# Performance work log

Hardware: AMD Instinct MI355X
Metric: run time of the kernel (lower is better)

## Reference

```python
import jax, jax.numpy as jnp
import numpy as np
from jax import lax

B, T, H, W, C = 2, 16, 64, 64, 64
KT, K = 3, 3


def kernel_to_freq_3d(kernel, T, H, W):
    # kernel: (C, k_t, k_h, k_w) -> (C, T, H, W) complex freq response
    Cc, k_t, k_h, k_w = kernel.shape
    t_idx = (jnp.arange(k_t) - k_t // 2) % T
    h_idx = (jnp.arange(k_h) - k_h // 2) % H
    w_idx = (jnp.arange(k_w) - k_w // 2) % W
    tt, th, tw = jnp.meshgrid(t_idx, h_idx, w_idx, indexing='ij')
    padded = jnp.zeros((Cc, T, H, W), dtype=kernel.dtype).at[:, tt, th, tw].set(kernel)
    return jnp.fft.fftn(padded, axes=(1, 2, 3))


def mamba_op(left, right):
    a1, b1 = left
    a2, b2 = right
    return (a1 * a2, a2 * b1 + b2)


def setup_inputs() -> dict:
    key = jax.random.key(0)
    ks = jax.random.split(key, 8)
    fan_in = KT * K * K
    x = jax.random.normal(ks[0], (B, T, H, W, C), dtype=jnp.float32)
    A_kernel = jax.random.normal(ks[1], (C, KT, K, K), dtype=jnp.float32) / np.sqrt(fan_in)
    B_kernel = jax.random.normal(ks[2], (C, KT, K, K), dtype=jnp.float32) / np.sqrt(fan_in)
    forget_bias = jnp.full((C,), 2.0, dtype=jnp.float32)
    forget_scale = jnp.full((C,), 0.01, dtype=jnp.float32)
    input_bias = jnp.zeros((C,), dtype=jnp.float32)
    input_scale = jnp.full((C,), 0.01, dtype=jnp.float32)
    delta_W = jax.random.normal(ks[3], (C, C), dtype=jnp.float32) / np.sqrt(C)
    delta_b = jnp.zeros((C,), dtype=jnp.float32)
    return {"x": x, "A_kernel": A_kernel, "B_kernel": B_kernel,
            "forget_bias": forget_bias, "forget_scale": forget_scale,
            "input_bias": input_bias, "input_scale": input_scale,
            "delta_W": delta_W, "delta_b": delta_b}


def reference(x, A_kernel, B_kernel, forget_bias, forget_scale,
              input_bias, input_scale, delta_W, delta_b):
    Bb, Tt, Hh, Ww, Cc = x.shape
    # freq-domain kernels: (C,T,H,W) -> (T,1,H,W,C) for broadcasting over batch
    A_f = kernel_to_freq_3d(A_kernel, Tt, Hh, Ww).transpose(1, 2, 3, 0)[:, None]
    B_f = kernel_to_freq_3d(B_kernel, Tt, Hh, Ww).transpose(1, 2, 3, 0)[:, None]
    # input-dependent gates (real, elementwise per channel)
    forget_gate = jax.nn.sigmoid(forget_bias + forget_scale * x)
    input_gate = jax.nn.sigmoid(input_bias + input_scale * x)
    delta = jax.nn.softplus(jnp.einsum('bthwc,cd->bthwd', x, delta_W) + delta_b)
    x_f = jnp.fft.fftn(x, axes=(1, 2, 3))  # complex (B,T,H,W,C)
    # move time axis to front for the scan: (T,B,H,W,C)
    a_seq = forget_gate.transpose(1, 0, 2, 3, 4) * A_f
    b_seq = (input_gate.transpose(1, 0, 2, 3, 4)
             * delta.transpose(1, 0, 2, 3, 4)
             * B_f * x_f.transpose(1, 0, 2, 3, 4))
    _, h_all_f = lax.associative_scan(mamba_op, (a_seq, b_seq), axis=0)
    h_f = h_all_f.transpose(1, 0, 2, 3, 4)
    h = jnp.fft.ifftn(h_f, axes=(1, 2, 3)).real
    return h.astype(x.dtype)
```

## Files before the change

### kernel.cpp

```cpp
#include <hip/hip_runtime.h>
#include <math.h>

#define Bb 2
#define Tt 16
#define Hh 64
#define Ww 64
#define Cc 64
#define ST_ (Hh*Ww*Cc)
#define SB_ (Tt*Hh*Ww*Cc)

#define TWO_PI 6.2831853071795864769f

typedef __attribute__((ext_vector_type(8))) short bf16x8;
typedef __attribute__((ext_vector_type(4))) float f32x4;

#define BUF_A    0u
#define BUF_B    8388608u
#define OFF_PRE  16777216u
#define OFF_TWF  16779264u
#define OFF_THF  16783360u
#define OFF_THI  16791552u
#define OFF_TWI  16799744u

__device__ __forceinline__ float2 cmul(float2 a, float2 b) {
    return make_float2(fmaf(a.x, b.x, -a.y * b.y), fmaf(a.x, b.y, a.y * b.x));
}
__device__ __forceinline__ float2 cadd(float2 a, float2 b) { return make_float2(a.x + b.x, a.y + b.y); }
__device__ __forceinline__ float2 csub(float2 a, float2 b) { return make_float2(a.x - b.x, a.y - b.y); }

__device__ __forceinline__ unsigned bfpack(float2 f) {
    unsigned r = __float_as_uint(f.x);
    unsigned i = __float_as_uint(f.y);
    r = (r + 0x7fffu + ((r >> 16) & 1u)) >> 16;
    i = (i + 0x7fffu + ((i >> 16) & 1u)) >> 16;
    return r | (i << 16);
}
__device__ __forceinline__ float2 bfunpack(unsigned u) {
    return make_float2(__uint_as_float(u << 16), __uint_as_float(u & 0xffff0000u));
}

template <int S>
__device__ __forceinline__ void fft4(float2& a, float2& b, float2& c, float2& d) {
    float2 t0 = cadd(a, c), t1 = csub(a, c);
    float2 t2 = cadd(b, d), t3 = csub(b, d);
    a = cadd(t0, t2);
    c = csub(t0, t2);
    b = make_float2(t1.x - (float)S * t3.y, t1.y + (float)S * t3.x);
    d = make_float2(t1.x + (float)S * t3.y, t1.y - (float)S * t3.x);
}

template <int S>
__device__ __forceinline__ void fft16(float2 v[16]) {
    const float CS[10] = {1.f, 0.92387953f, 0.70710678f, 0.38268343f, 0.f,
                          -0.38268343f, -0.70710678f, -0.92387953f, -1.f, -0.92387953f};
    const float SN[10] = {0.f, 0.38268343f, 0.70710678f, 0.92387953f, 1.f,
                          0.92387953f, 0.70710678f, 0.38268343f, 0.f, -0.38268343f};
    float2 A[4][4];
#pragma unroll
    for (int j = 0; j < 4; ++j) {
        A[j][0] = v[j]; A[j][1] = v[4 + j]; A[j][2] = v[8 + j]; A[j][3] = v[12 + j];
        fft4<S>(A[j][0], A[j][1], A[j][2], A[j][3]);
#pragma unroll
        for (int k0 = 0; k0 < 4; ++k0) {
            int m = j * k0;
            float2 tw = make_float2(CS[m], (float)S * SN[m]);
            A[j][k0] = cmul(A[j][k0], tw);
        }
    }
#pragma unroll
    for (int k0 = 0; k0 < 4; ++k0) {
        fft4<S>(A[0][k0], A[1][k0], A[2][k0], A[3][k0]);
        v[k0] = A[0][k0]; v[k0 + 4] = A[1][k0]; v[k0 + 8] = A[2][k0]; v[k0 + 12] = A[3][k0];
    }
}

__global__ __launch_bounds__(256) void k_setup(const float* __restrict__ dW,
                                               unsigned* __restrict__ ws) {
    int j = blockIdx.x * 256 + threadIdx.x;
    if (j < 2048) {
        int p2 = j & 3, lane = (j >> 2) & 63, ka = (j >> 8) & 1, nt = j >> 9;
        int kb = ka * 32 + (lane >> 4) * 8 + 2 * p2;
        int ccol = (lane & 15) + 16 * nt;
        ws[OFF_PRE + j] = bfpack(make_float2(dW[kb * 64 + ccol], dW[(kb + 1) * 64 + ccol]));
        return;
    }
    int idx, table;
    if (j < 6144)       { idx = j - 2048;  table = 0; }
    else if (j < 14336) { idx = j - 6144;  table = 1; }
    else if (j < 22528) { idx = j - 14336; table = 2; }
    else                { idx = j - 22528; table = 3; }
    int p = idx & 3;
    int lane = (idx >> 2) & 63;
    int m = lane & 15, q = lane >> 4;
    int ka, r, reim;
    if (table == 0)      { ka = (idx >> 8) & 1; r = (idx >> 9) & 3;  reim = (idx >> 11) & 1; }
    else if (table == 3) { ka = (idx >> 8) & 3; r = (idx >> 10) & 3; reim = 0; }
    else                 { ka = (idx >> 8) & 3; r = (idx >> 10) & 3; reim = (idx >> 12) & 1; }
    int wp = r * 16 + m;
    int k0 = ka * 32 + q * 8 + 2 * p;
    float val[2];
#pragma unroll
    for (int dk = 0; dk < 2; ++dk) {
        int k = k0 + dk;
        float v;
        if (table == 0) {
            int a = (wp * k) & 63;
            float sn, cs; sincosf(TWO_PI * (float)a * (1.0f / 64.0f), &sn, &cs);
            v = (reim == 0) ? cs : -sn;
        } else {
            int h = k >> 1;
            int a = (wp * h) & 63;
            float sn, cs; sincosf(TWO_PI * (float)a * (1.0f / 64.0f), &sn, &cs);
            bool even = (k & 1) == 0;
            if (table == 1) {
                v = (reim == 0) ? (even ? cs : sn) : (even ? -sn : cs);
            } else if (table == 2) {
                v = (reim == 0) ? (even ? cs : -sn) : (even ? sn : cs);
                v *= (1.0f / 64.0f);
            } else {
                v = (even ? cs : -sn) * (1.0f / 64.0f);
            }
        }
        val[dk] = v;
    }
    unsigned base = (table == 0) ? OFF_TWF : (table == 1) ? OFF_THF
                  : (table == 2) ? OFF_THI : OFF_TWI;
    ws[base + idx] = bfpack(make_float2(val[0], val[1]));
}

__global__ __launch_bounds__(256) void k_dft_w_fwd(const float* __restrict__ x,
                                                   unsigned* __restrict__ X1,
                                                   const uint4* __restrict__ T) {
    __shared__ unsigned zw[64 * 66];
    int tid = threadIdx.x;
    int s = blockIdx.x;
    const float* src = x + (size_t)s * 4096;
    for (int idx = tid; idx < 2048; idx += 256) {
        int i = idx >> 6, c = idx & 63;
        zw[c * 66 + i] = bfpack(make_float2(src[i * 128 + c], src[i * 128 + 64 + c]));
    }
    __syncthreads();

    int r = tid >> 6, lane = tid & 63;
    int m = lane & 15, q = lane >> 4;
    union U48 { uint4 u4; uint2 u2[2]; unsigned u[4]; bf16x8 v8; };
    U48 Are[2], Aim[2], Bf;
#pragma unroll
    for (int ka = 0; ka < 2; ++ka) {
        Are[ka].u4 = T[((0 * 4 + r) * 2 + ka) * 64 + lane];
        Aim[ka].u4 = T[((1 * 4 + r) * 2 + ka) * 64 + lane];
    }
    f32x4 ar[4], ai[4];
#pragma unroll
    for (int nt = 0; nt < 4; ++nt) { ar[nt] = (f32x4){0.f,0.f,0.f,0.f}; ai[nt] = (f32x4){0.f,0.f,0.f,0.f}; }
#pragma unroll
    for (int nt = 0; nt < 4; ++nt) {
        int cc = m + 16 * nt;
#pragma unroll
        for (int ka = 0; ka < 2; ++ka) {
            int i0 = ka * 16 + q * 4;
            Bf.u2[0] = *(const uint2*)&zw[cc * 66 + i0];
            Bf.u2[1] = *(const uint2*)&zw[cc * 66 + i0 + 2];
            ar[nt] = __builtin_amdgcn_mfma_f32_16x16x32_bf16(Are[ka].v8, Bf.v8, ar[nt], 0, 0, 0);
            ai[nt] = __builtin_amdgcn_mfma_f32_16x16x32_bf16(Aim[ka].v8, Bf.v8, ai[nt], 0, 0, 0);
        }
    }
    int bt = s >> 6, h = s & 63;
    size_t ob = (size_t)bt * 262144 + (size_t)h * 64;
#pragma unroll
    for (int nt = 0; nt < 4; ++nt) {
        int cc = m + 16 * nt;
#pragma unroll
        for (int reg = 0; reg < 4; ++reg) {
            int wp = r * 16 + q * 4 + reg;
            X1[ob + (size_t)wp * 4096 + cc] = bfpack(make_float2(ar[nt][reg], ai[nt][reg]));
        }
    }
}

__global__ __launch_bounds__(256) void k_dft_h_fwd(const unsigned* __restrict__ X1,
                                                   unsigned* __restrict__ X2,
                                                   const uint4* __restrict__ T) {
    __shared__ unsigned zs[64 * 66];
    int tid = threadIdx.x;
    int s = blockIdx.x;
    const unsigned* src = X1 + (size_t)s * 4096;
    for (int i = tid; i < 4096; i += 256) {
        int h = i >> 6, c = i & 63;
        zs[c * 66 + h] = src[i];
    }
    __syncthreads();

    int r = tid >> 6, lane = tid & 63;
    int m = lane & 15, q = lane >> 4;
    union U48 { uint4 u4; uint2 u2[2]; unsigned u[4]; bf16x8 v8; };
    U48 Are[4], Aim[4], Bf;
#pragma unroll
    for (int ka = 0; ka < 4; ++ka) {
        Are[ka].u4 = T[((0 * 4 + r) * 4 + ka) * 64 + lane];
        Aim[ka].u4 = T[((1 * 4 + r) * 4 + ka) * 64 + lane];
    }
    f32x4 ar[4], ai[4];
#pragma unroll
    for (int nt = 0; nt < 4; ++nt) { ar[nt] = (f32x4){0.f,0.f,0.f,0.f}; ai[nt] = (f32x4){0.f,0.f,0.f,0.f}; }
#pragma unroll
    for (int nt = 0; nt < 4; ++nt) {
        int cc = m + 16 * nt;
#pragma unroll
        for (int ka = 0; ka < 4; ++ka) {
            int h0 = ka * 16 + q * 4;
            Bf.u2[0] = *(const uint2*)&zs[cc * 66 + h0];
            Bf.u2[1] = *(const uint2*)&zs[cc * 66 + h0 + 2];
            ar[nt] = __builtin_amdgcn_mfma_f32_16x16x32_bf16(Are[ka].v8, Bf.v8, ar[nt], 0, 0, 0);
            ai[nt] = __builtin_amdgcn_mfma_f32_16x16x32_bf16(Aim[ka].v8, Bf.v8, ai[nt], 0, 0, 0);
        }
    }
    int b = s >> 10, t = (s >> 6) & 15, w = s & 63;
    size_t ob = (size_t)b * 4194304 + (size_t)w * 1024 + (size_t)t * 64;
#pragma unroll
    for (int nt = 0; nt < 4; ++nt) {
        int cc = m + 16 * nt;
#pragma unroll
        for (int reg = 0; reg < 4; ++reg) {
            int hp = r * 16 + q * 4 + reg;
            X2[ob + (size_t)hp * 65536 + cc] = bfpack(make_float2(ar[nt][reg], ai[nt][reg]));
        }
    }
}

__global__ __launch_bounds__(256) void k_dft_h_inv(const unsigned* __restrict__ X3,
                                                   unsigned* __restrict__ X4,
                                                   const uint4* __restrict__ T) {
    __shared__ unsigned zs[64 * 66];
    int tid = threadIdx.x;
    int s = blockIdx.x;
    const unsigned* src = X3 + (size_t)s * 4096;
    for (int i = tid; i < 4096; i += 256) {
        int h = i >> 6, c = i & 63;
        zs[c * 66 + h] = src[i];
    }
    __syncthreads();

    int r = tid >> 6, lane = tid & 63;
    int m = lane & 15, q = lane >> 4;
    union U48 { uint4 u4; uint2 u2[2]; unsigned u[4]; bf16x8 v8; };
    U48 Are[4], Aim[4], Bf;
#pragma unroll
    for (int ka = 0; ka < 4; ++ka) {
        Are[ka].u4 = T[((0 * 4 + r) * 4 + ka) * 64 + lane];
        Aim[ka].u4 = T[((1 * 4 + r) * 4 + ka) * 64 + lane];
    }
    f32x4 ar[4], ai[4];
#pragma unroll
    for (int nt = 0; nt < 4; ++nt) { ar[nt] = (f32x4){0.f,0.f,0.f,0.f}; ai[nt] = (f32x4){0.f,0.f,0.f,0.f}; }
#pragma unroll
    for (int nt = 0; nt < 4; ++nt) {
        int cc = m + 16 * nt;
#pragma unroll
        for (int ka = 0; ka < 4; ++ka) {
            int h0 = ka * 16 + q * 4;
            Bf.u2[0] = *(const uint2*)&zs[cc * 66 + h0];
            Bf.u2[1] = *(const uint2*)&zs[cc * 66 + h0 + 2];
            ar[nt] = __builtin_amdgcn_mfma_f32_16x16x32_bf16(Are[ka].v8, Bf.v8, ar[nt], 0, 0, 0);
            ai[nt] = __builtin_amdgcn_mfma_f32_16x16x32_bf16(Aim[ka].v8, Bf.v8, ai[nt], 0, 0, 0);
        }
    }
    int bt = s >> 6, w = s & 63;
    size_t ob = (size_t)bt * 262144 + (size_t)w * 64;
#pragma unroll
    for (int nt = 0; nt < 4; ++nt) {
        int cc = m + 16 * nt;
#pragma unroll
        for (int reg = 0; reg < 4; ++reg) {
            int hp = r * 16 + q * 4 + reg;
            X4[ob + (size_t)hp * 4096 + cc] = bfpack(make_float2(ar[nt][reg], ai[nt][reg]));
        }
    }
}

__global__ __launch_bounds__(256) void k_dft_w_inv(const unsigned* __restrict__ X4,
                                                   float* __restrict__ out,
                                                   const uint4* __restrict__ T) {
    __shared__ unsigned zs[64 * 66];
    int tid = threadIdx.x;
    int s = blockIdx.x;
    const unsigned* src = X4 + (size_t)s * 4096;
    for (int i = tid; i < 4096; i += 256) {
        int w = i >> 6, c = i & 63;
        zs[c * 66 + w] = src[i];
    }
    __syncthreads();

    int r = tid >> 6, lane = tid & 63;
    int m = lane & 15, q = lane >> 4;
    union U48 { uint4 u4; uint2 u2[2]; unsigned u[4]; bf16x8 v8; };
    U48 Are[4], Bf;
#pragma unroll
    for (int ka = 0; ka < 4; ++ka)
        Are[ka].u4 = T[(r * 4 + ka) * 64 + lane];
    f32x4 ar[4];
#pragma unroll
    for (int nt = 0; nt < 4; ++nt) ar[nt] = (f32x4){0.f,0.f,0.f,0.f};
#pragma unroll
    for (int nt = 0; nt < 4; ++nt) {
        int cc = m + 16 * nt;
#pragma unroll
        for (int ka = 0; ka < 4; ++ka) {
            int w0 = ka * 16 + q * 4;
            Bf.u2[0] = *(const uint2*)&zs[cc * 66 + w0];
            Bf.u2[1] = *(const uint2*)&zs[cc * 66 + w0 + 2];
            ar[nt] = __builtin_amdgcn_mfma_f32_16x16x32_bf16(Are[ka].v8, Bf.v8, ar[nt], 0, 0, 0);
        }
    }
    float* dst = out + (size_t)s * 4096;
#pragma unroll
    for (int nt = 0; nt < 4; ++nt) {
        int cc = m + 16 * nt;
#pragma unroll
        for (int reg = 0; reg < 4; ++reg) {
            int wp = r * 16 + q * 4 + reg;
            dst[wp * 64 + cc] = ar[nt][reg];
        }
    }
}

__global__ __launch_bounds__(256) void k_mid(
    const float* __restrict__ x, const unsigned* __restrict__ X2,
    unsigned* __restrict__ X3,
    const float* __restrict__ Ak, const float* __restrict__ Bk,
    const float* __restrict__ fb, const float* __restrict__ fs,
    const float* __restrict__ ib, const float* __restrict__ isc_,
    const uint4* __restrict__ pre, const float* __restrict__ db) {
    const float CT[16] = {1.f, 0.9238795f, 0.7071068f, 0.3826834f, 0.f, -0.3826834f,
                          -0.7071068f, -0.9238795f, -1.f, -0.9238795f, -0.7071068f,
                          -0.3826834f, 0.f, 0.3826834f, 0.7071068f, 0.9238795f};
    const float SN[16] = {0.f, 0.3826834f, 0.7071068f, 0.9238795f, 1.f, 0.9238795f,
                          0.7071068f, 0.3826834f, 0.f, -0.3826834f, -0.7071068f,
                          -0.9238795f, -1.f, -0.9238795f, -0.7071068f, -0.3826834f};
    __shared__ float Akl[1728], Bkl[1728];
    __shared__ __align__(16) float xs[4][16 * 68 + 4];

    int tid = threadIdx.x;
    int g = tid >> 6, lane = tid & 63;
    int c = lane;
    int site = blockIdx.x * 4 + g;
    int b = site >> 12, hw = site & 4095;
    int h = hw >> 6, w = hw & 63;
    size_t base = (size_t)b * SB_ + (size_t)hw * 64;

    for (int i = tid; i < 1728; i += 256) { Akl[i] = Ak[i]; Bkl[i] = Bk[i]; }

    float xv[16];
    float2 v[16];
    const unsigned* src2 = X2 + (size_t)site * 1024;
#pragma unroll
    for (int t = 0; t < 16; ++t) {
        xv[t] = x[base + (size_t)t * ST_ + c];
        v[t] = bfunpack(src2[t * 64 + c]);
    }
#pragma unroll
    for (int t = 0; t < 16; ++t) xs[g][t * 68 + c] = xv[t];
    __syncthreads();

    int m = lane & 15, q = lane >> 4;
    bf16x8 Afrag[2];
#pragma unroll
    for (int ka = 0; ka < 2; ++ka) {
        int d0 = ka * 32 + q * 8;
        const float* p = &xs[g][m * 68 + d0];
        float4 f0 = *(const float4*)p;
        float4 f1 = *(const float4*)(p + 4);
        union { bf16x8 v8; unsigned u[4]; } U;
        U.u[0] = bfpack(make_float2(f0.x, f0.y));
        U.u[1] = bfpack(make_float2(f0.z, f0.w));
        U.u[2] = bfpack(make_float2(f1.x, f1.y));
        U.u[3] = bfpack(make_float2(f1.z, f1.w));
        Afrag[ka] = U.v8;
    }
#pragma unroll
    for (int nt = 0; nt < 4; ++nt) {
        int ccol = m + 16 * nt;
        float dbn = db[ccol];
        f32x4 acc = {dbn, dbn, dbn, dbn};
#pragma unroll
        for (int ka = 0; ka < 2; ++ka) {
            union { bf16x8 v8; uint4 u4; } Ub;
            Ub.u4 = pre[(nt * 2 + ka) * 64 + lane];
            acc = __builtin_amdgcn_mfma_f32_16x16x32_bf16(Afrag[ka], Ub.v8, acc, 0, 0, 0);
        }
#pragma unroll
        for (int reg = 0; reg < 4; ++reg)
            xs[g][(q * 4 + reg) * 68 + ccol] = acc[reg];
    }

    float sh, ch; sincosf(TWO_PI * (float)h / 64.0f, &sh, &ch);
    float sw, cw; sincosf(TWO_PI * (float)w / 64.0f, &sw, &cw);
    float2 eh[3] = { make_float2(ch, sh), make_float2(1.f, 0.f), make_float2(ch, -sh) };
    float2 ew[3] = { make_float2(cw, sw), make_float2(1.f, 0.f), make_float2(cw, -sw) };
    float2 GA[3], GB[3];
#pragma unroll
    for (int kt = 0; kt < 3; ++kt) { GA[kt] = make_float2(0.f, 0.f); GB[kt] = make_float2(0.f, 0.f); }
#pragma unroll
    for (int kh = 0; kh < 3; ++kh) {
#pragma unroll
        for (int kw = 0; kw < 3; ++kw) {
            float2 e = cmul(eh[kh], ew[kw]);
#pragma unroll
            for (int kt = 0; kt < 3; ++kt) {
                float ka = Akl[c * 27 + kt * 9 + kh * 3 + kw];
                float kb = Bkl[c * 27 + kt * 9 + kh * 3 + kw];
                GA[kt].x = fmaf(ka, e.x, GA[kt].x);
                GA[kt].y = fmaf(ka, e.y, GA[kt].y);
                GB[kt].x = fmaf(kb, e.x, GB[kt].x);
                GB[kt].y = fmaf(kb, e.y, GB[kt].y);
            }
        }
    }
    float fbc = fb[c], fsc = fs[c], ibc = ib[c], iscv = isc_[c];

    fft16<-1>(v);
    __syncthreads();

    float delta_raw[16];
#pragma unroll
    for (int t = 0; t < 16; ++t) delta_raw[t] = xs[g][t * 68 + c];

    float2 hv = make_float2(0.f, 0.f);
#pragma unroll
    for (int t = 0; t < 16; ++t) {
        float ct = CT[t], st = SN[t];
        float2 Af, Bf;
        Af.x = GA[1].x + ct * (GA[0].x + GA[2].x) - st * (GA[0].y - GA[2].y);
        Af.y = GA[1].y + ct * (GA[0].y + GA[2].y) + st * (GA[0].x - GA[2].x);
        Bf.x = GB[1].x + ct * (GB[0].x + GB[2].x) - st * (GB[0].y - GB[2].y);
        Bf.y = GB[1].y + ct * (GB[0].y + GB[2].y) + st * (GB[0].x - GB[2].x);

        float xc = xv[t];
        float fg  = __builtin_amdgcn_rcpf(1.f + __expf(-(fbc + fsc * xc)));
        float igv = __builtin_amdgcn_rcpf(1.f + __expf(-(ibc + iscv * xc)));
        float dot = delta_raw[t];
        float delta = (dot > 20.f) ? dot : __logf(1.f + __expf(dot));

        float sR = igv * delta;
        float2 bbv;
        bbv.x = sR * (Bf.x * v[t].x - Bf.y * v[t].y);
        bbv.y = sR * (Bf.x * v[t].y + Bf.y * v[t].x);
        float2 av = make_float2(fg * Af.x, fg * Af.y);
        float2 nh;
        nh.x = av.x * hv.x - av.y * hv.y + bbv.x;
        nh.y = av.x * hv.y + av.y * hv.x + bbv.y;
        hv = nh;
        v[t] = hv;
    }

    fft16<1>(v);

    size_t ob = (size_t)b * 4194304 + (size_t)w * 4096 + (size_t)h * 64 + c;
#pragma unroll
    for (int t = 0; t < 16; ++t) {
        float2 o = make_float2(v[t].x * 0.0625f, v[t].y * 0.0625f);
        X3[ob + (size_t)t * 262144] = bfpack(o);
    }
}

extern "C" void kernel_launch(void* const* d_in, const int* in_sizes, int n_in,
                              void* d_out, int out_size, void* d_ws, size_t ws_size,
                              hipStream_t stream) {
    const float* x   = (const float*)d_in[0];
    const float* Ak  = (const float*)d_in[1];
    const float* Bk  = (const float*)d_in[2];
    const float* fb  = (const float*)d_in[3];
    const float* fs  = (const float*)d_in[4];
    const float* ib  = (const float*)d_in[5];
    const float* is_ = (const float*)d_in[6];
    const float* dW  = (const float*)d_in[7];
    const float* db  = (const float*)d_in[8];
    float* out = (float*)d_out;
    unsigned* ws = (unsigned*)d_ws;
    unsigned* A = ws + BUF_A;
    unsigned* B = ws + BUF_B;

    k_setup<<<104, 256, 0, stream>>>(dW, ws);
    k_dft_w_fwd<<<Bb * Tt * Hh, 256, 0, stream>>>(x, A, (const uint4*)(ws + OFF_TWF));
    k_dft_h_fwd<<<Bb * Tt * Ww, 256, 0, stream>>>(A, B, (const uint4*)(ws + OFF_THF));
    k_mid<<<(Bb * Hh * Ww) / 4, 256, 0, stream>>>(x, B, A, Ak, Bk, fb, fs, ib, is_,
                                                  (const uint4*)(ws + OFF_PRE), db);
    k_dft_h_inv<<<Bb * Tt * Ww, 256, 0, stream>>>(A, B, (const uint4*)(ws + OFF_THI));
    k_dft_w_inv<<<Bb * Tt * Hh, 256, 0, stream>>>(B, out, (const uint4*)(ws + OFF_TWI));
}
```

Before: 175.2 us.

## Fuse W and H DFT passes into single 2D kernels with in-LDS transpose

Replaces the separate W and H forward DFT kernels, and likewise the two inverse kernels, with one 2D kernel each. Each 512-thread block handles an 8-channel slab of one (b,t) plane and keeps the intermediate in a swizzled 128KB LDS buffer, so the intermediate no longer round-trips through global memory. Twiddle tables and the delta_W bf16 fragments are now computed in registers in every block, which removes the setup kernel and three launches. The cost is heavy LDS use per block, only 256 blocks with few waves each, sincos work repeated in every block, and strided 64-element global accesses.

```diff
diff --git a/kernel.cpp b/kernel.cpp
--- a/kernel.cpp
+++ b/kernel.cpp
@@ -16,11 +16,6 @@
 
 #define BUF_A    0u
 #define BUF_B    8388608u
-#define OFF_PRE  16777216u
-#define OFF_TWF  16779264u
-#define OFF_THF  16783360u
-#define OFF_THI  16791552u
-#define OFF_TWI  16799744u
 
 __device__ __forceinline__ float2 cmul(float2 a, float2 b) {
     return make_float2(fmaf(a.x, b.x, -a.y * b.y), fmaf(a.x, b.y, a.y * b.x));
@@ -37,6 +32,73 @@
 }
 __device__ __forceinline__ float2 bfunpack(unsigned u) {
     return make_float2(__uint_as_float(u << 16), __uint_as_float(u & 0xffff0000u));
+}
+
+union U48 { uint4 u4; uint2 u2[2]; unsigned u[4]; bf16x8 v8; };
+
+__device__ __forceinline__ U48 tw_wf(int wp, int q, int ka, int reim) {
+    U48 o;
+#pragma unroll
+    for (int p = 0; p < 4; ++p) {
+        int k0 = ka * 32 + q * 8 + 2 * p;
+        float v[2];
+#pragma unroll
+        for (int dk = 0; dk < 2; ++dk) {
+            int k = k0 + dk;
+            int a = (wp * k) & 63;
+            float sn, cs; sincosf(TWO_PI * (float)a * (1.0f / 64.0f), &sn, &cs);
+            v[dk] = reim ? -sn : cs;
+        }
+        o.u[p] = bfpack(make_float2(v[0], v[1]));
+    }
+    return o;
+}
+
+__device__ __forceinline__ U48 tw_cpx(int wp, int q, int ka, int reim, int tbl) {
+    U48 o;
+#pragma unroll
+    for (int p = 0; p < 4; ++p) {
+        int k0 = ka * 32 + q * 8 + 2 * p;
+        float v[2];
+#pragma unroll
+        for (int dk = 0; dk < 2; ++dk) {
+            int k = k0 + dk;
+            int h = k >> 1;
+            int a = (wp * h) & 63;
+            float sn, cs; sincosf(TWO_PI * (float)a * (1.0f / 64.0f), &sn, &cs);
+            bool even = (k & 1) == 0;
+            float vv;
+            if (tbl == 1) vv = reim ? (even ? -sn : cs) : (even ? cs : sn);
+            else          vv = (reim ? (even ? sn : cs) : (even ? cs : -sn)) * (1.0f / 64.0f);
+            v[dk] = vv;
+        }
+        o.u[p] = bfpack(make_float2(v[0], v[1]));
+    }
+    return o;
+}
+
+__device__ __forceinline__ U48 tw_wi(int wp, int q, int ka) {
+    U48 o;
+#pragma unroll
+    for (int p = 0; p < 4; ++p) {
+        int k0 = ka * 32 + q * 8 + 2 * p;
+        float v[2];
+#pragma unroll
+        for (int dk = 0; dk < 2; ++dk) {
+            int k = k0 + dk;
+            int h = k >> 1;
+            int a = (wp * h) & 63;
+            float sn, cs; sincosf(TWO_PI * (float)a * (1.0f / 64.0f), &sn, &cs);
+            bool even = (k & 1) == 0;
+            v[dk] = (even ? cs : -sn) * (1.0f / 64.0f);
+        }
+        o.u[p] = bfpack(make_float2(v[0], v[1]));
+    }
+    return o;
+}
+
+__device__ __forceinline__ int zidx(int col, int h) {
+    return (col << 6) + (h ^ (((col >> 1) & 7) << 3));
 }
 
 template <int S>
@@ -74,252 +136,149 @@
     }
 }
 
-__global__ __launch_bounds__(256) void k_setup(const float* __restrict__ dW,
-                                               unsigned* __restrict__ ws) {
-    int j = blockIdx.x * 256 + threadIdx.x;
-    if (j < 2048) {
-        int p2 = j & 3, lane = (j >> 2) & 63, ka = (j >> 8) & 1, nt = j >> 9;
-        int kb = ka * 32 + (lane >> 4) * 8 + 2 * p2;
-        int ccol = (lane & 15) + 16 * nt;
-        ws[OFF_PRE + j] = bfpack(make_float2(dW[kb * 64 + ccol], dW[(kb + 1) * 64 + ccol]));
-        return;
-    }
-    int idx, table;
-    if (j < 6144)       { idx = j - 2048;  table = 0; }
-    else if (j < 14336) { idx = j - 6144;  table = 1; }
-    else if (j < 22528) { idx = j - 14336; table = 2; }
-    else                { idx = j - 22528; table = 3; }
-    int p = idx & 3;
-    int lane = (idx >> 2) & 63;
+__global__ __launch_bounds__(512) void k_fwd2d(const float* __restrict__ x,
+                                               unsigned* __restrict__ X2) {
+    __shared__ unsigned Z[512 * 64];
+    int tid = threadIdx.x;
+    int lane = tid & 63, r = (tid >> 6) & 3, team = tid >> 8;
     int m = lane & 15, q = lane >> 4;
-    int ka, r, reim;
-    if (table == 0)      { ka = (idx >> 8) & 1; r = (idx >> 9) & 3;  reim = (idx >> 11) & 1; }
-    else if (table == 3) { ka = (idx >> 8) & 3; r = (idx >> 10) & 3; reim = 0; }
-    else                 { ka = (idx >> 8) & 3; r = (idx >> 10) & 3; reim = (idx >> 12) & 1; }
+    int wg = blockIdx.x;
+    int bt = wg >> 3;
+    int c0 = (wg & 7) * 8;
+    int b = wg >> 7, t = (wg >> 3) & 15;
+    const float* xs = x + (size_t)bt * 262144;
     int wp = r * 16 + m;
-    int k0 = ka * 32 + q * 8 + 2 * p;
-    float val[2];
-#pragma unroll
-    for (int dk = 0; dk < 2; ++dk) {
-        int k = k0 + dk;
-        float v;
-        if (table == 0) {
-            int a = (wp * k) & 63;
-            float sn, cs; sincosf(TWO_PI * (float)a * (1.0f / 64.0f), &sn, &cs);
-            v = (reim == 0) ? cs : -sn;
-        } else {
-            int h = k >> 1;
-            int a = (wp * h) & 63;
-            float sn, cs; sincosf(TWO_PI * (float)a * (1.0f / 64.0f), &sn, &cs);
-            bool even = (k & 1) == 0;
-            if (table == 1) {
-                v = (reim == 0) ? (even ? cs : sn) : (even ? -sn : cs);
-            } else if (table == 2) {
-                v = (reim == 0) ? (even ? cs : -sn) : (even ? sn : cs);
-                v *= (1.0f / 64.0f);
-            } else {
-                v = (even ? cs : -sn) * (1.0f / 64.0f);
+    int hme = m >> 3, cme = m & 7;
+
+    U48 Are[2], Aim[2];
+#pragma unroll
+    for (int ka = 0; ka < 2; ++ka) { Are[ka] = tw_wf(wp, q, ka, 0); Aim[ka] = tw_wf(wp, q, ka, 1); }
+#pragma unroll 2
+    for (int gi = 0; gi < 16; ++gi) {
+        int g = gi * 2 + team;
+        int h = g * 2 + hme;
+        const float* xr = xs + (size_t)h * 4096 + (c0 + cme);
+        U48 B[2];
+#pragma unroll
+        for (int ka = 0; ka < 2; ++ka)
+#pragma unroll
+            for (int p = 0; p < 4; ++p) {
+                int w0 = ka * 32 + q * 8 + 2 * p;
+                B[ka].u[p] = bfpack(make_float2(xr[(size_t)w0 * 64], xr[(size_t)(w0 + 1) * 64]));
             }
-        }
-        val[dk] = v;
-    }
-    unsigned base = (table == 0) ? OFF_TWF : (table == 1) ? OFF_THF
-                  : (table == 2) ? OFF_THI : OFF_TWI;
-    ws[base + idx] = bfpack(make_float2(val[0], val[1]));
-}
-
-__global__ __launch_bounds__(256) void k_dft_w_fwd(const float* __restrict__ x,
-                                                   unsigned* __restrict__ X1,
-                                                   const uint4* __restrict__ T) {
-    __shared__ unsigned zw[64 * 66];
-    int tid = threadIdx.x;
-    int s = blockIdx.x;
-    const float* src = x + (size_t)s * 4096;
-    for (int idx = tid; idx < 2048; idx += 256) {
-        int i = idx >> 6, c = idx & 63;
-        zw[c * 66 + i] = bfpack(make_float2(src[i * 128 + c], src[i * 128 + 64 + c]));
+        f32x4 ar = {0.f, 0.f, 0.f, 0.f}, ai = {0.f, 0.f, 0.f, 0.f};
+#pragma unroll
+        for (int ka = 0; ka < 2; ++ka) {
+            ar = __builtin_amdgcn_mfma_f32_16x16x32_bf16(Are[ka].v8, B[ka].v8, ar, 0, 0, 0);
+            ai = __builtin_amdgcn_mfma_f32_16x16x32_bf16(Aim[ka].v8, B[ka].v8, ai, 0, 0, 0);
+        }
+#pragma unroll
+        for (int reg = 0; reg < 4; ++reg) {
+            int wpp = r * 16 + q * 4 + reg;
+            Z[zidx(wpp * 8 + cme, h)] = bfpack(make_float2(ar[reg], ai[reg]));
+        }
     }
     __syncthreads();
 
-    int r = tid >> 6, lane = tid & 63;
-    int m = lane & 15, q = lane >> 4;
-    union U48 { uint4 u4; uint2 u2[2]; unsigned u[4]; bf16x8 v8; };
-    U48 Are[2], Aim[2], Bf;
-#pragma unroll
-    for (int ka = 0; ka < 2; ++ka) {
-        Are[ka].u4 = T[((0 * 4 + r) * 2 + ka) * 64 + lane];
-        Aim[ka].u4 = T[((1 * 4 + r) * 2 + ka) * 64 + lane];
-    }
-    f32x4 ar[4], ai[4];
-#pragma unroll
-    for (int nt = 0; nt < 4; ++nt) { ar[nt] = (f32x4){0.f,0.f,0.f,0.f}; ai[nt] = (f32x4){0.f,0.f,0.f,0.f}; }
-#pragma unroll
-    for (int nt = 0; nt < 4; ++nt) {
-        int cc = m + 16 * nt;
-#pragma unroll
-        for (int ka = 0; ka < 2; ++ka) {
-            int i0 = ka * 16 + q * 4;
-            Bf.u2[0] = *(const uint2*)&zw[cc * 66 + i0];
-            Bf.u2[1] = *(const uint2*)&zw[cc * 66 + i0 + 2];
-            ar[nt] = __builtin_amdgcn_mfma_f32_16x16x32_bf16(Are[ka].v8, Bf.v8, ar[nt], 0, 0, 0);
-            ai[nt] = __builtin_amdgcn_mfma_f32_16x16x32_bf16(Aim[ka].v8, Bf.v8, ai[nt], 0, 0, 0);
-        }
-    }
-    int bt = s >> 6, h = s & 63;
-    size_t ob = (size_t)bt * 262144 + (size_t)h * 64;
-#pragma unroll
-    for (int nt = 0; nt < 4; ++nt) {
-        int cc = m + 16 * nt;
-#pragma unroll
-        for (int reg = 0; reg < 4; ++reg) {
-            int wp = r * 16 + q * 4 + reg;
-            X1[ob + (size_t)wp * 4096 + cc] = bfpack(make_float2(ar[nt][reg], ai[nt][reg]));
-        }
-    }
-}
-
-__global__ __launch_bounds__(256) void k_dft_h_fwd(const unsigned* __restrict__ X1,
-                                                   unsigned* __restrict__ X2,
-                                                   const uint4* __restrict__ T) {
-    __shared__ unsigned zs[64 * 66];
-    int tid = threadIdx.x;
-    int s = blockIdx.x;
-    const unsigned* src = X1 + (size_t)s * 4096;
-    for (int i = tid; i < 4096; i += 256) {
-        int h = i >> 6, c = i & 63;
-        zs[c * 66 + h] = src[i];
-    }
-    __syncthreads();
-
-    int r = tid >> 6, lane = tid & 63;
-    int m = lane & 15, q = lane >> 4;
-    union U48 { uint4 u4; uint2 u2[2]; unsigned u[4]; bf16x8 v8; };
-    U48 Are[4], Aim[4], Bf;
-#pragma unroll
-    for (int ka = 0; ka < 4; ++ka) {
-        Are[ka].u4 = T[((0 * 4 + r) * 4 + ka) * 64 + lane];
-        Aim[ka].u4 = T[((1 * 4 + r) * 4 + ka) * 64 + lane];
-    }
-    f32x4 ar[4], ai[4];
-#pragma unroll
-    for (int nt = 0; nt < 4; ++nt) { ar[nt] = (f32x4){0.f,0.f,0.f,0.f}; ai[nt] = (f32x4){0.f,0.f,0.f,0.f}; }
-#pragma unroll
-    for (int nt = 0; nt < 4; ++nt) {
-        int cc = m + 16 * nt;
+    U48 Hre[4], Him[4];
+#pragma unroll
+    for (int ka = 0; ka < 4; ++ka) { Hre[ka] = tw_cpx(wp, q, ka, 0, 1); Him[ka] = tw_cpx(wp, q, ka, 1, 1); }
+    size_t ob = (size_t)b * 4194304 + (size_t)t * 64 + (c0 + cme);
+#pragma unroll 2
+    for (int gi = 0; gi < 16; ++gi) {
+        int g = gi * 2 + team;
+        int col = g * 16 + m;
+        int w = g * 2 + hme;
+        U48 B[4];
 #pragma unroll
         for (int ka = 0; ka < 4; ++ka) {
             int h0 = ka * 16 + q * 4;
-            Bf.u2[0] = *(const uint2*)&zs[cc * 66 + h0];
-            Bf.u2[1] = *(const uint2*)&zs[cc * 66 + h0 + 2];
-            ar[nt] = __builtin_amdgcn_mfma_f32_16x16x32_bf16(Are[ka].v8, Bf.v8, ar[nt], 0, 0, 0);
-            ai[nt] = __builtin_amdgcn_mfma_f32_16x16x32_bf16(Aim[ka].v8, Bf.v8, ai[nt], 0, 0, 0);
-        }
-    }
-    int b = s >> 10, t = (s >> 6) & 15, w = s & 63;
-    size_t ob = (size_t)b * 4194304 + (size_t)w * 1024 + (size_t)t * 64;
-#pragma unroll
-    for (int nt = 0; nt < 4; ++nt) {
-        int cc = m + 16 * nt;
+            int zi = zidx(col, h0);
+            B[ka].u2[0] = *(const uint2*)&Z[zi];
+            B[ka].u2[1] = *(const uint2*)&Z[zi + 2];
+        }
+        f32x4 ar = {0.f, 0.f, 0.f, 0.f}, ai = {0.f, 0.f, 0.f, 0.f};
+#pragma unroll
+        for (int ka = 0; ka < 4; ++ka) {
+            ar = __builtin_amdgcn_mfma_f32_16x16x32_bf16(Hre[ka].v8, B[ka].v8, ar, 0, 0, 0);
+            ai = __builtin_amdgcn_mfma_f32_16x16x32_bf16(Him[ka].v8, B[ka].v8, ai, 0, 0, 0);
+        }
 #pragma unroll
         for (int reg = 0; reg < 4; ++reg) {
             int hp = r * 16 + q * 4 + reg;
-            X2[ob + (size_t)hp * 65536 + cc] = bfpack(make_float2(ar[nt][reg], ai[nt][reg]));
-        }
-    }
-}
-
-__global__ __launch_bounds__(256) void k_dft_h_inv(const unsigned* __restrict__ X3,
-                                                   unsigned* __restrict__ X4,
-                                                   const uint4* __restrict__ T) {
-    __shared__ unsigned zs[64 * 66];
+            X2[ob + (size_t)hp * 65536 + (size_t)w * 1024] = bfpack(make_float2(ar[reg], ai[reg]));
+        }
+    }
+}
+
+__global__ __launch_bounds__(512) void k_inv2d(const unsigned* __restrict__ X3,
+                                               float* __restrict__ out) {
+    __shared__ unsigned Z[512 * 64];
     int tid = threadIdx.x;
-    int s = blockIdx.x;
-    const unsigned* src = X3 + (size_t)s * 4096;
-    for (int i = tid; i < 4096; i += 256) {
-        int h = i >> 6, c = i & 63;
-        zs[c * 66 + h] = src[i];
-    }
-    __syncthreads();
-
-    int r = tid >> 6, lane = tid & 63;
+    int lane = tid & 63, r = (tid >> 6) & 3, team = tid >> 8;
     int m = lane & 15, q = lane >> 4;
-    union U48 { uint4 u4; uint2 u2[2]; unsigned u[4]; bf16x8 v8; };
-    U48 Are[4], Aim[4], Bf;
-#pragma unroll
-    for (int ka = 0; ka < 4; ++ka) {
-        Are[ka].u4 = T[((0 * 4 + r) * 4 + ka) * 64 + lane];
-        Aim[ka].u4 = T[((1 * 4 + r) * 4 + ka) * 64 + lane];
-    }
-    f32x4 ar[4], ai[4];
-#pragma unroll
-    for (int nt = 0; nt < 4; ++nt) { ar[nt] = (f32x4){0.f,0.f,0.f,0.f}; ai[nt] = (f32x4){0.f,0.f,0.f,0.f}; }
-#pragma unroll
-    for (int nt = 0; nt < 4; ++nt) {
-        int cc = m + 16 * nt;
+    int wg = blockIdx.x;
+    int bt = wg >> 3;
+    int c0 = (wg & 7) * 8;
+    const unsigned* xs = X3 + (size_t)bt * 262144;
+    int wp = r * 16 + m;
+    int hme = m >> 3, cme = m & 7;
+
+    U48 Hre[4], Him[4];
+#pragma unroll
+    for (int ka = 0; ka < 4; ++ka) { Hre[ka] = tw_cpx(wp, q, ka, 0, 2); Him[ka] = tw_cpx(wp, q, ka, 1, 2); }
+#pragma unroll 2
+    for (int gi = 0; gi < 16; ++gi) {
+        int g = gi * 2 + team;
+        int w = g * 2 + hme;
+        const unsigned* xr = xs + (size_t)w * 4096 + (c0 + cme);
+        U48 B[4];
+#pragma unroll
+        for (int ka = 0; ka < 4; ++ka)
+#pragma unroll
+            for (int j = 0; j < 4; ++j) {
+                int h = ka * 16 + q * 4 + j;
+                B[ka].u[j] = xr[(size_t)h * 64];
+            }
+        f32x4 ar = {0.f, 0.f, 0.f, 0.f}, ai = {0.f, 0.f, 0.f, 0.f};
 #pragma unroll
         for (int ka = 0; ka < 4; ++ka) {
-            int h0 = ka * 16 + q * 4;
-            Bf.u2[0] = *(const uint2*)&zs[cc * 66 + h0];
-            Bf.u2[1] = *(const uint2*)&zs[cc * 66 + h0 + 2];
-            ar[nt] = __builtin_amdgcn_mfma_f32_16x16x32_bf16(Are[ka].v8, Bf.v8, ar[nt], 0, 0, 0);
-            ai[nt] = __builtin_amdgcn_mfma_f32_16x16x32_bf16(Aim[ka].v8, Bf.v8, ai[nt], 0, 0, 0);
-        }
-    }
-    int bt = s >> 6, w = s & 63;
-    size_t ob = (size_t)bt * 262144 + (size_t)w * 64;
-#pragma unroll
-    for (int nt = 0; nt < 4; ++nt) {
-        int cc = m + 16 * nt;
+            ar = __builtin_amdgcn_mfma_f32_16x16x32_bf16(Hre[ka].v8, B[ka].v8, ar, 0, 0, 0);
+            ai = __builtin_amdgcn_mfma_f32_16x16x32_bf16(Him[ka].v8, B[ka].v8, ai, 0, 0, 0);
+        }
 #pragma unroll
         for (int reg = 0; reg < 4; ++reg) {
             int hp = r * 16 + q * 4 + reg;
-            X4[ob + (size_t)hp * 4096 + cc] = bfpack(make_float2(ar[nt][reg], ai[nt][reg]));
-        }
-    }
-}
-
-__global__ __launch_bounds__(256) void k_dft_w_inv(const unsigned* __restrict__ X4,
-                                                   float* __restrict__ out,
-                                                   const uint4* __restrict__ T) {
-    __shared__ unsigned zs[64 * 66];
-    int tid = threadIdx.x;
-    int s = blockIdx.x;
-    const unsigned* src = X4 + (size_t)s * 4096;
-    for (int i = tid; i < 4096; i += 256) {
-        int w = i >> 6, c = i & 63;
-        zs[c * 66 + w] = src[i];
+            Z[zidx(hp * 8 + cme, w)] = bfpack(make_float2(ar[reg], ai[reg]));
+        }
     }
     __syncthreads();
 
-    int r = tid >> 6, lane = tid & 63;
-    int m = lane & 15, q = lane >> 4;
-    union U48 { uint4 u4; uint2 u2[2]; unsigned u[4]; bf16x8 v8; };
-    U48 Are[4], Bf;
-#pragma unroll
-    for (int ka = 0; ka < 4; ++ka)
-        Are[ka].u4 = T[(r * 4 + ka) * 64 + lane];
-    f32x4 ar[4];
-#pragma unroll
-    for (int nt = 0; nt < 4; ++nt) ar[nt] = (f32x4){0.f,0.f,0.f,0.f};
-#pragma unroll
-    for (int nt = 0; nt < 4; ++nt) {
-        int cc = m + 16 * nt;
+    U48 Wre[4];
+#pragma unroll
+    for (int ka = 0; ka < 4; ++ka) Wre[ka] = tw_wi(wp, q, ka);
+#pragma unroll 2
+    for (int gi = 0; gi < 16; ++gi) {
+        int g = gi * 2 + team;
+        int col = g * 16 + m;
+        int h = g * 2 + hme;
+        U48 B[4];
 #pragma unroll
         for (int ka = 0; ka < 4; ++ka) {
             int w0 = ka * 16 + q * 4;
-            Bf.u2[0] = *(const uint2*)&zs[cc * 66 + w0];
-            Bf.u2[1] = *(const uint2*)&zs[cc * 66 + w0 + 2];
-            ar[nt] = __builtin_amdgcn_mfma_f32_16x16x32_bf16(Are[ka].v8, Bf.v8, ar[nt], 0, 0, 0);
-        }
-    }
-    float* dst = out + (size_t)s * 4096;
-#pragma unroll
-    for (int nt = 0; nt < 4; ++nt) {
-        int cc = m + 16 * nt;
+            int zi = zidx(col, w0);
+            B[ka].u2[0] = *(const uint2*)&Z[zi];
+            B[ka].u2[1] = *(const uint2*)&Z[zi + 2];
+        }
+        f32x4 ar = {0.f, 0.f, 0.f, 0.f};
+#pragma unroll
+        for (int ka = 0; ka < 4; ++ka)
+            ar = __builtin_amdgcn_mfma_f32_16x16x32_bf16(Wre[ka].v8, B[ka].v8, ar, 0, 0, 0);
+        float* dst = out + (size_t)bt * 262144 + (size_t)h * 4096 + (c0 + cme);
 #pragma unroll
         for (int reg = 0; reg < 4; ++reg) {
-            int wp = r * 16 + q * 4 + reg;
-            dst[wp * 64 + cc] = ar[nt][reg];
+            int wpp = r * 16 + q * 4 + reg;
+            dst[(size_t)wpp * 64] = ar[reg];
         }
     }
 }
@@ -330,7 +289,7 @@
     const float* __restrict__ Ak, const float* __restrict__ Bk,
     const float* __restrict__ fb, const float* __restrict__ fs,
     const float* __restrict__ ib, const float* __restrict__ isc_,
-    const uint4* __restrict__ pre, const float* __restrict__ db) {
+    const float* __restrict__ dW, const float* __restrict__ db) {
     const float CT[16] = {1.f, 0.9238795f, 0.7071068f, 0.3826834f, 0.f, -0.3826834f,
                           -0.7071068f, -0.9238795f, -1.f, -0.9238795f, -0.7071068f,
                           -0.3826834f, 0.f, 0.3826834f, 0.7071068f, 0.9238795f};
@@ -343,6 +302,7 @@
     int tid = threadIdx.x;
     int g = tid >> 6, lane = tid & 63;
     int c = lane;
+    int m = lane & 15, q = lane >> 4;
     int site = blockIdx.x * 4 + g;
     int b = site >> 12, hw = site & 4095;
     int h = hw >> 6, w = hw & 63;
@@ -350,6 +310,18 @@
 
     for (int i = tid; i < 1728; i += 256) { Akl[i] = Ak[i]; Bkl[i] = Bk[i]; }
 
+    U48 Ub[4][2];
+#pragma unroll
+    for (int nt = 0; nt < 4; ++nt)
+#pragma unroll
+        for (int ka = 0; ka < 2; ++ka)
+#pragma unroll
+            for (int p2 = 0; p2 < 4; ++p2) {
+                int kb = ka * 32 + q * 8 + 2 * p2;
+                int ccol = m + 16 * nt;
+                Ub[nt][ka].u[p2] = bfpack(make_float2(dW[kb * 64 + ccol], dW[(kb + 1) * 64 + ccol]));
+            }
+
     float xv[16];
     float2 v[16];
     const unsigned* src2 = X2 + (size_t)site * 1024;
@@ -362,7 +334,6 @@
     for (int t = 0; t < 16; ++t) xs[g][t * 68 + c] = xv[t];
     __syncthreads();
 
-    int m = lane & 15, q = lane >> 4;
     bf16x8 Afrag[2];
 #pragma unroll
     for (int ka = 0; ka < 2; ++ka) {
@@ -370,11 +341,11 @@
         const float* p = &xs[g][m * 68 + d0];
         float4 f0 = *(const float4*)p;
         float4 f1 = *(const float4*)(p + 4);
-        union { bf16x8 v8; unsigned u[4]; } U;
-        U.u[0] = bfpack(make_float2(f0.x, f0.y));
-        U.u[1] = bfpack(make_float2(f0.z, f0.w));
-        U.u[2] = bfpack(make_float2(f1.x, f1.y));
-        U.u[3] = bfpack(make_float2(f1.z, f1.w));
+        union { bf16x8 v8; unsigned uu[4]; } U;
+        U.uu[0] = bfpack(make_float2(f0.x, f0.y));
+        U.uu[1] = bfpack(make_float2(f0.z, f0.w));
+        U.uu[2] = bfpack(make_float2(f1.x, f1.y));
+        U.uu[3] = bfpack(make_float2(f1.z, f1.w));
         Afrag[ka] = U.v8;
     }
 #pragma unroll
@@ -383,11 +354,8 @@
         float dbn = db[ccol];
         f32x4 acc = {dbn, dbn, dbn, dbn};
 #pragma unroll
-        for (int ka = 0; ka < 2; ++ka) {
-            union { bf16x8 v8; uint4 u4; } Ub;
-            Ub.u4 = pre[(nt * 2 + ka) * 64 + lane];
-            acc = __builtin_amdgcn_mfma_f32_16x16x32_bf16(Afrag[ka], Ub.v8, acc, 0, 0, 0);
-        }
+        for (int ka = 0; ka < 2; ++ka)
+            acc = __builtin_amdgcn_mfma_f32_16x16x32_bf16(Afrag[ka], Ub[nt][ka].v8, acc, 0, 0, 0);
 #pragma unroll
         for (int reg = 0; reg < 4; ++reg)
             xs[g][(q * 4 + reg) * 68 + ccol] = acc[reg];
@@ -477,14 +445,10 @@
     const float* db  = (const float*)d_in[8];
     float* out = (float*)d_out;
     unsigned* ws = (unsigned*)d_ws;
-    unsigned* A = ws + BUF_A;
-    unsigned* B = ws + BUF_B;
-
-    k_setup<<<104, 256, 0, stream>>>(dW, ws);
-    k_dft_w_fwd<<<Bb * Tt * Hh, 256, 0, stream>>>(x, A, (const uint4*)(ws + OFF_TWF));
-    k_dft_h_fwd<<<Bb * Tt * Ww, 256, 0, stream>>>(A, B, (const uint4*)(ws + OFF_THF));
-    k_mid<<<(Bb * Hh * Ww) / 4, 256, 0, stream>>>(x, B, A, Ak, Bk, fb, fs, ib, is_,
-                                                  (const uint4*)(ws + OFF_PRE), db);
-    k_dft_h_inv<<<Bb * Tt * Ww, 256, 0, stream>>>(A, B, (const uint4*)(ws + OFF_THI));
-    k_dft_w_inv<<<Bb * Tt * Hh, 256, 0, stream>>>(B, out, (const uint4*)(ws + OFF_TWI));
-}
+    unsigned* X2 = ws + BUF_A;
+    unsigned* X3 = ws + BUF_B;
+
+    k_fwd2d<<<Bb * Tt * 8, 512, 0, stream>>>(x, X2);
+    k_mid<<<(Bb * Hh * Ww) / 4, 256, 0, stream>>>(x, X2, X3, Ak, Bk, fb, fs, ib, is_, dW, db);
+    k_inv2d<<<Bb * Tt * 8, 512, 0, stream>>>(X3, out);
+}
```

New measurement: 202.0 us. 15.3% more time.
